# Optimization experiments

Hardware: AMD Instinct MI355X
Metric: run time of the kernel (lower is better)

Reference implementation:

```python
import jax, jax.numpy as jnp
import numpy as np
from jax import lax

PC_RANGE = (-54.0, -54.0, -5.0, 54.0, 54.0, 3.0)
HEIGHTS = (-1.0, 0.0, 1.0)  # all within [z_min, z_max]
IMG_H, IMG_W = 256.0, 704.0  # batch_input_shape of the camera image
BN_EPS = 1e-5


def setup_inputs() -> dict:
    key = jax.random.key(0)
    ks = jax.random.split(key, 11)
    d = {}
    d['radar_bev'] = jax.random.normal(ks[0], (2, 384, 180, 180), jnp.float32)
    d['img_feat'] = jax.random.normal(ks[1], (2, 256, 64, 176), jnp.float32)
    d['lidar2img'] = jax.random.normal(ks[2], (2, 3, 4), jnp.float32)
    d['w1'] = jax.random.normal(ks[3], (384, 256, 1, 1), jnp.float32) * 0.05
    d['bn1'] = jax.random.uniform(ks[4], (4, 384), jnp.float32, 0.1, 1.0)
    d['w2'] = jax.random.normal(ks[5], (384, 384, 3, 3), jnp.float32) * 0.02
    d['bn2'] = jax.random.uniform(ks[6], (4, 384), jnp.float32, 0.1, 1.0)
    d['wf1'] = jax.random.normal(ks[7], (384, 768, 3, 3), jnp.float32) * 0.02
    d['bnf1'] = jax.random.uniform(ks[8], (4, 384), jnp.float32, 0.1, 1.0)
    d['wf2'] = jax.random.normal(ks[9], (384, 384, 3, 3), jnp.float32) * 0.02
    d['bnf2'] = jax.random.uniform(ks[10], (4, 384), jnp.float32, 0.1, 1.0)
    return d


def _conv(x, w, pad):
    return lax.conv_general_dilated(x, w, (1, 1), [(pad, pad), (pad, pad)],
                                    dimension_numbers=('NCHW', 'OIHW', 'NCHW'))


def _bn_relu(x, p):
    g, b, m, v = p[0], p[1], p[2], p[3]
    y = (x - m[:, None, None]) * (g[:, None, None] / jnp.sqrt(v[:, None, None] + BN_EPS)) + b[:, None, None]
    return jax.nn.relu(y)


def _bilinear_sample(img, gx, gy):
    # img: [C,H,W]; gx,gy: [N] normalized coords in grid_sample convention
    # (align_corners=False, padding_mode='zeros')
    C, H, W = img.shape
    ix = ((gx + 1.0) * W - 1.0) * 0.5
    iy = ((gy + 1.0) * H - 1.0) * 0.5
    x0 = jnp.floor(ix); y0 = jnp.floor(iy)
    wx1 = ix - x0; wx0 = 1.0 - wx1
    wy1 = iy - y0; wy0 = 1.0 - wy1

    def corner(xc, yc, w):
        inb = (xc >= 0) & (xc < W) & (yc >= 0) & (yc < H)
        xi = jnp.clip(xc, 0, W - 1).astype(jnp.int32)
        yi = jnp.clip(yc, 0, H - 1).astype(jnp.int32)
        return img[:, yi, xi] * (w * inb)[None, :]

    return (corner(x0, y0, wx0 * wy0) + corner(x0 + 1, y0, wx1 * wy0)
            + corner(x0, y0 + 1, wx0 * wy1) + corner(x0 + 1, y0 + 1, wx1 * wy1))


def reference(radar_bev, img_feat, lidar2img, w1, bn1, w2, bn2, wf1, bnf1, wf2, bnf2):
    B, _, bev_h, bev_w = radar_bev.shape
    x_min, y_min, z_min, x_max, y_max, z_max = PC_RANGE
    xs = jnp.linspace(x_min, x_max, bev_w + 1, dtype=jnp.float32)[:-1] + (x_max - x_min) / bev_w * 0.5
    ys = jnp.linspace(y_min, y_max, bev_h + 1, dtype=jnp.float32)[:-1] + (y_max - y_min) / bev_h * 0.5
    gy, gx = jnp.meshgrid(ys, xs, indexing='ij')  # [bev_h, bev_w]
    zs = jnp.asarray(HEIGHTS, jnp.float32)
    Z = zs.shape[0]
    # points: [Z, bev_h, bev_w, 4] -> [N, 4]
    pts = jnp.stack([jnp.broadcast_to(gx, (Z, bev_h, bev_w)),
                     jnp.broadcast_to(gy, (Z, bev_h, bev_w)),
                     jnp.broadcast_to(zs[:, None, None], (Z, bev_h, bev_w)),
                     jnp.ones((Z, bev_h, bev_w), jnp.float32)], axis=-1).reshape(-1, 4)
    # project: [B, N, 3]
    proj = jnp.einsum('nk,bjk->bnj', pts, lidar2img)
    depth = jnp.maximum(proj[:, :, 2], 1e-5)
    px = proj[:, :, 0] / depth
    py = proj[:, :, 1] / depth
    norm_x = px / IMG_W * 2.0 - 1.0
    norm_y = py / IMG_H * 2.0 - 1.0
    sampled = jax.vmap(_bilinear_sample)(img_feat, norm_x, norm_y)  # [B, C, N]
    valid = ((px >= 0) & (px < IMG_W) & (py >= 0) & (py < IMG_H)
             & (proj[:, :, 2] > 1e-5)).astype(jnp.float32)  # [B, N]
    C = img_feat.shape[1]
    sampled = sampled.reshape(B, C, Z, bev_h, bev_w)
    valid = valid.reshape(B, 1, Z, bev_h, bev_w)
    image_bev = (sampled * valid).sum(axis=2) / jnp.maximum(valid.sum(axis=2), 1.0)
    # image_bev_encoder: 1x1 conv -> BN -> ReLU -> 3x3 conv -> BN -> ReLU
    h = _bn_relu(_conv(image_bev, w1, 0), bn1)
    h = _bn_relu(_conv(h, w2, 1), bn2)
    # bev_fusion on concat(radar, image_bev)
    f = jnp.concatenate([radar_bev, h], axis=1)
    f = _bn_relu(_conv(f, wf1, 1), bnf1)
    f = _bn_relu(_conv(f, wf2, 1), bnf2)
    return f
```

## Files before the change

kernel.cpp:

```cpp
#include <hip/hip_runtime.h>
#include <hip/hip_bf16.h>

#define BEV 180
#define NPOS (BEV * BEV)
#define MTOT (2 * NPOS)
#define IH 64
#define IW 176
#define CIMG 256

typedef __attribute__((ext_vector_type(8))) short bf16x8;
typedef __attribute__((ext_vector_type(4))) float f32x4;

__device__ __forceinline__ void gload_lds16(const void* g, void* l) {
  __builtin_amdgcn_global_load_lds(
      (const __attribute__((address_space(1))) void*)g,
      (__attribute__((address_space(3))) void*)l, 16, 0, 0);
}

__global__ void k_zero(unsigned long long* p) { p[threadIdx.x] = 0ULL; }

template <typename OT>
__device__ __forceinline__ OT conv_out(float v);
template <>
__device__ __forceinline__ float conv_out<float>(float v) { return v; }
template <>
__device__ __forceinline__ __hip_bfloat16 conv_out<__hip_bfloat16>(float v) { return __float2bfloat16(v); }

template <typename OT>
__global__ void k_transpose(const float* __restrict__ in, OT* __restrict__ out, int R, int CL) {
  __shared__ float tile[32][33];
  const float* inb = in + (size_t)blockIdx.z * R * CL;
  OT* outb = out + (size_t)blockIdx.z * R * CL;
  int c0 = blockIdx.x * 32, r0 = blockIdx.y * 32;
  int tx = threadIdx.x, ty = threadIdx.y;
#pragma unroll
  for (int i = 0; i < 32; i += 8) {
    int r = r0 + ty + i, c = c0 + tx;
    tile[ty + i][tx] = (r < R && c < CL) ? inb[(size_t)r * CL + c] : 0.f;
  }
  __syncthreads();
#pragma unroll
  for (int i = 0; i < 32; i += 8) {
    int c = c0 + ty + i, r = r0 + tx;
    if (c < CL && r < R) outb[(size_t)c * R + r] = conv_out<OT>(tile[tx][ty + i]);
  }
}

__global__ void k_sample(const float* __restrict__ imgT, const float* __restrict__ l2i,
                         __hip_bfloat16* __restrict__ out) {
  int blk = blockIdx.x;
  int b = blk / NPOS, rem = blk - b * NPOS;
  int hy = rem / BEV, wx = rem - hy * BEV;
  int c = threadIdx.x;
  float gx = -54.f + 0.3f + 0.6f * (float)wx;
  float gy = -54.f + 0.3f + 0.6f * (float)hy;
  const float* L = l2i + b * 12;
  const float* img = imgT + (size_t)b * (IH * IW * CIMG);
  float acc = 0.f, vcnt = 0.f;
#pragma unroll
  for (int zi = 0; zi < 3; ++zi) {
    float z = (float)(zi - 1);
    float p0 = L[0] * gx + L[1] * gy + L[2] * z + L[3];
    float p1 = L[4] * gx + L[5] * gy + L[6] * z + L[7];
    float p2 = L[8] * gx + L[9] * gy + L[10] * z + L[11];
    float d = fmaxf(p2, 1e-5f);
    float px = p0 / d, py = p1 / d;
    if (px >= 0.f && px < 704.f && py >= 0.f && py < 256.f && p2 > 1e-5f) {
      vcnt += 1.f;
      float ix = px * 0.25f - 0.5f, iy = py * 0.25f - 0.5f;
      float xf = floorf(ix), yf = floorf(iy);
      float wx1 = ix - xf, wy1 = iy - yf;
      float wx0 = 1.f - wx1, wy0 = 1.f - wy1;
      int x0 = (int)xf, y0 = (int)yf;
      int x1 = x0 + 1, y1 = y0 + 1;
      bool bx0 = (unsigned)x0 < IW, bx1 = (unsigned)x1 < IW;
      bool by0 = (unsigned)y0 < IH, by1 = (unsigned)y1 < IH;
      float s = 0.f;
      if (bx0 && by0) s += wx0 * wy0 * img[((size_t)y0 * IW + x0) * CIMG + c];
      if (bx1 && by0) s += wx1 * wy0 * img[((size_t)y0 * IW + x1) * CIMG + c];
      if (bx0 && by1) s += wx0 * wy1 * img[((size_t)y1 * IW + x0) * CIMG + c];
      if (bx1 && by1) s += wx1 * wy1 * img[((size_t)y1 * IW + x1) * CIMG + c];
      acc += s;
    }
  }
  out[(size_t)blk * CIMG + c] = __float2bfloat16(acc / fmaxf(vcnt, 1.f));
}

__global__ void k_packw(const float* __restrict__ w, __hip_bfloat16* __restrict__ wp,
                        int Co, int Ci, int T) {
  size_t idx = (size_t)blockIdx.x * 256 + threadIdx.x;
  size_t tot = (size_t)Co * Ci * T;
  if (idx >= tot) return;
  int ci = (int)(idx % Ci);
  size_t r = idx / Ci;
  int co = (int)(r % Co);
  int tap = (int)(r / Co);
  wp[idx] = __float2bfloat16(w[((size_t)co * Ci + ci) * T + tap]);
}

__global__ void k_packbn(const float* __restrict__ bn, float* __restrict__ sb, int C) {
  int i = blockIdx.x * blockDim.x + threadIdx.x;
  if (i >= C) return;
  float g = bn[i], b = bn[C + i], m = bn[2 * C + i], v = bn[3 * C + i];
  float s = g / sqrtf(v + 1e-5f);
  sb[i] = s;
  sb[C + i] = b - m * s;
}

__global__ __launch_bounds__(256, 2) void k_conv(
    const __hip_bfloat16* __restrict__ x0, const __hip_bfloat16* __restrict__ x1,
    int cin0, int cin1,
    const __hip_bfloat16* __restrict__ wp, const float* __restrict__ sb,
    int taps, int isFinal,
    __hip_bfloat16* __restrict__ obf, float* __restrict__ of32,
    const __hip_bfloat16* __restrict__ zp) {
  const int Cout = 384;
  __shared__ __hip_bfloat16 As[352 * 64];
  __shared__ __hip_bfloat16 Bs[2][128 * 64];
  const int t = threadIdx.x;
  const int w = t >> 6, l = t & 63;
  const int bid = blockIdx.x;
  const int b = bid / 144;
  const int rr = bid - b * 144;
  const int y0 = (rr / 12) * 16;
  const int x0c = (rr - (rr / 12) * 12) * 16;
  const int n0 = blockIdx.y * 128;
  const int cinTot = cin0 + cin1;
  const size_t tapStride = (size_t)Cout * cinTot * 2;
  const int nA0 = cin0 >> 6, nA1 = cin1 >> 6, nA = nA0 + nA1;
  const int P = nA * taps;

  const int baseRow = t >> 3;
  const int cb = ((t & 7) ^ (baseRow & 7)) * 16;
  int posIdx[11];
  unsigned okMask = 0;
#pragma unroll
  for (int j = 0; j < 11; ++j) {
    int row = j * 32 + baseRow;
    int yy = row / 18, xx = row - yy * 18;
    int ys = y0 - 1 + yy, xg = x0c - 1 + xx;
    if (row < 324 && (unsigned)ys < 180u && (unsigned)xg < 180u) okMask |= (1u << j);
    posIdx[j] = b * NPOS + ys * BEV + xg;
  }
  size_t bOff[4];
#pragma unroll
  for (int j = 0; j < 4; ++j)
    bOff[j] = (size_t)(n0 + j * 32 + baseRow) * (size_t)(cinTot * 2) + (size_t)cb;

  auto issueA = [&](int kc) {
    int s1 = (kc >= nA0);
    int kcw = kc - (s1 ? nA0 : 0);
    const char* xb = s1 ? (const char*)x1 : (const char*)x0;
    size_t cinB = (size_t)(s1 ? cin1 : cin0) * 2;
    size_t ko = (size_t)kcw * 128 + (size_t)cb;
    char* dst = (char*)As + w * 1024;
#pragma unroll
    for (int j = 0; j < 11; ++j) {
      const char* src = ((okMask >> j) & 1) ? (xb + (size_t)posIdx[j] * cinB + ko)
                                            : (const char*)zp;
      gload_lds16(src, dst + j * 4096);
    }
  };
  auto issueB = [&](int q, int kc, int tq) {
    int s1 = (kc >= nA0);
    int kcw = kc - (s1 ? nA0 : 0);
    int segoff = s1 ? cin0 : 0;
    const char* wt = (const char*)wp + (size_t)tq * tapStride + (size_t)(segoff + kcw * 64) * 2;
    char* dst = (char*)Bs[q & 1] + w * 1024;
#pragma unroll
    for (int j = 0; j < 4; ++j) gload_lds16(wt + bOff[j], dst + j * 4096);
  };

  f32x4 acc[8][4];
#pragma unroll
  for (int mi = 0; mi < 8; ++mi)
#pragma unroll
    for (int ni = 0; ni < 4; ++ni) acc[mi][ni] = f32x4{0.f, 0.f, 0.f, 0.f};

  const int wq = w >> 1;
  const int wn = (w & 1) * 64;
  const int xl = l & 15, kq = l >> 4;

  issueA(0);
  issueB(0, 0, 0);

  int kc = 0, tap = 0;
  for (int p = 0; p < P; ++p) {
    if (p + 1 < P) {
      int tq = tap + 1, kn = kc;
      if (tq == taps) { tq = 0; ++kn; }
      issueB(p + 1, kn, tq);
      asm volatile("s_waitcnt vmcnt(4)" ::: "memory");
    } else {
      asm volatile("s_waitcnt vmcnt(0)" ::: "memory");
    }
    __builtin_amdgcn_s_barrier();
    asm volatile("" ::: "memory");

    const int dy = (taps == 9) ? (tap / 3 - 1) : 0;
    const int dx = (taps == 9) ? (tap - (tap / 3) * 3 - 1) : 0;
    const int sRow0 = (wq * 8 + dy + 1) * 18 + xl + dx + 1;
    const char* bLds = (const char*)Bs[p & 1];
    __builtin_amdgcn_s_setprio(1);
#pragma unroll
    for (int ks = 0; ks < 2; ++ks) {
      const int g = ks * 4 + kq;
      bf16x8 af[8], bfr[4];
#pragma unroll
      for (int mi = 0; mi < 8; ++mi) {
        int s = sRow0 + mi * 18;
        af[mi] = *(const bf16x8*)((const char*)As + s * 128 + ((g ^ (s & 7)) * 16));
      }
#pragma unroll
      for (int ni = 0; ni < 4; ++ni) {
        int rB = wn + ni * 16 + xl;
        bfr[ni] = *(const bf16x8*)(bLds + rB * 128 + ((g ^ (rB & 7)) * 16));
      }
#pragma unroll
      for (int mi = 0; mi < 8; ++mi)
#pragma unroll
        for (int ni = 0; ni < 4; ++ni)
          acc[mi][ni] = __builtin_amdgcn_mfma_f32_16x16x32_bf16(af[mi], bfr[ni], acc[mi][ni], 0, 0, 0);
    }
    __builtin_amdgcn_s_setprio(0);
    asm volatile("" ::: "memory");
    __builtin_amdgcn_s_barrier();

    if (tap == taps - 1 && kc + 1 < nA) issueA(kc + 1);
    if (++tap == taps) { tap = 0; ++kc; }
  }

  float sc[4], bi[4];
#pragma unroll
  for (int ni = 0; ni < 4; ++ni) {
    int cc = n0 + wn + ni * 16 + xl;
    sc[ni] = sb[cc];
    bi[ni] = sb[Cout + cc];
  }
#pragma unroll
  for (int mi = 0; mi < 8; ++mi) {
    int y = y0 + wq * 8 + mi;
    if (y >= BEV) continue;
#pragma unroll
    for (int j = 0; j < 4; ++j) {
      int x = x0c + kq * 4 + j;
      if (x >= BEV) continue;
      int pp = b * NPOS + y * BEV + x;
#pragma unroll
      for (int ni = 0; ni < 4; ++ni) {
        int cc = n0 + wn + ni * 16 + xl;
        float v = fmaxf(acc[mi][ni][j] * sc[ni] + bi[ni], 0.f);
        if (isFinal) {
          of32[((size_t)(b * Cout + cc)) * NPOS + (size_t)y * BEV + x] = v;
        } else {
          obf[(size_t)pp * Cout + cc] = __float2bfloat16(v);
        }
      }
    }
  }
}

extern "C" void kernel_launch(void* const* d_in, const int* in_sizes, int n_in,
                              void* d_out, int out_size, void* d_ws, size_t ws_size,
                              hipStream_t stream) {
  const float* radar = (const float*)d_in[0];
  const float* imgf = (const float*)d_in[1];
  const float* l2i = (const float*)d_in[2];
  const float* w1 = (const float*)d_in[3];
  const float* bn1 = (const float*)d_in[4];
  const float* w2 = (const float*)d_in[5];
  const float* bn2 = (const float*)d_in[6];
  const float* wf1 = (const float*)d_in[7];
  const float* bnf1 = (const float*)d_in[8];
  const float* wf2 = (const float*)d_in[9];
  const float* bnf2 = (const float*)d_in[10];

  char* ws = (char*)d_ws;
  size_t off = 0;
  auto alloc = [&](size_t bytes) {
    char* p = ws + off;
    off += (bytes + 255) & ~(size_t)255;
    return p;
  };
  char* zp = alloc(4096);
  char* imgT = alloc((size_t)2 * IH * IW * CIMG * 4);
  char* ibev = alloc((size_t)MTOT * CIMG * 2);
  char* radarT = imgT;
  char* h1 = alloc((size_t)MTOT * 384 * 2);
  char* h2 = alloc((size_t)MTOT * 384 * 2);
  char* f1 = h1;
  char* wp1 = alloc((size_t)1 * 384 * 256 * 2);
  char* wp2 = alloc((size_t)9 * 384 * 384 * 2);
  char* wpf1 = alloc((size_t)9 * 384 * 768 * 2);
  char* wpf2 = alloc((size_t)9 * 384 * 384 * 2);
  char* sb1 = alloc(2 * 384 * 4);
  char* sb2 = alloc(2 * 384 * 4);
  char* sbf1 = alloc(2 * 384 * 4);
  char* sbf2 = alloc(2 * 384 * 4);

  k_zero<<<1, 512, 0, stream>>>((unsigned long long*)zp);

  dim3 tb(32, 8);
  k_transpose<float><<<dim3((IH * IW + 31) / 32, (CIMG + 31) / 32, 2), tb, 0, stream>>>(
      imgf, (float*)imgT, CIMG, IH * IW);

  auto packw = [&](const float* src, char* dst, int Co, int Ci, int T) {
    size_t tot = (size_t)Co * Ci * T;
    k_packw<<<(unsigned)((tot + 255) / 256), 256, 0, stream>>>(src, (__hip_bfloat16*)dst, Co, Ci, T);
  };
  packw(w1, wp1, 384, 256, 1);
  packw(w2, wp2, 384, 384, 9);
  packw(wf1, wpf1, 384, 768, 9);
  packw(wf2, wpf2, 384, 384, 9);
  k_packbn<<<2, 256, 0, stream>>>(bn1, (float*)sb1, 384);
  k_packbn<<<2, 256, 0, stream>>>(bn2, (float*)sb2, 384);
  k_packbn<<<2, 256, 0, stream>>>(bnf1, (float*)sbf1, 384);
  k_packbn<<<2, 256, 0, stream>>>(bnf2, (float*)sbf2, 384);

  k_sample<<<MTOT, 256, 0, stream>>>((const float*)imgT, l2i, (__hip_bfloat16*)ibev);

  dim3 cg(288, 3);
  k_conv<<<cg, 256, 0, stream>>>((const __hip_bfloat16*)ibev, nullptr, 256, 0,
                                 (const __hip_bfloat16*)wp1, (const float*)sb1, 1, 0,
                                 (__hip_bfloat16*)h1, nullptr, (const __hip_bfloat16*)zp);
  k_transpose<__hip_bfloat16><<<dim3((NPOS + 31) / 32, (384 + 31) / 32, 2), tb, 0, stream>>>(
      radar, (__hip_bfloat16*)radarT, 384, NPOS);
  k_conv<<<cg, 256, 0, stream>>>((const __hip_bfloat16*)h1, nullptr, 384, 0,
                                 (const __hip_bfloat16*)wp2, (const float*)sb2, 9, 0,
                                 (__hip_bfloat16*)h2, nullptr, (const __hip_bfloat16*)zp);
  k_conv<<<cg, 256, 0, stream>>>((const __hip_bfloat16*)radarT, (const __hip_bfloat16*)h2, 384, 384,
                                 (const __hip_bfloat16*)wpf1, (const float*)sbf1, 9, 0,
                                 (__hip_bfloat16*)f1, nullptr, (const __hip_bfloat16*)zp);
  k_conv<<<cg, 256, 0, stream>>>((const __hip_bfloat16*)f1, nullptr, 384, 0,
                                 (const __hip_bfloat16*)wpf2, (const float*)sbf2, 9, 1,
                                 nullptr, (float*)d_out, (const __hip_bfloat16*)zp);
}
```

Baseline: 940.0 us.

## Use bf16 image features and cut per-iteration barriers in conv pipeline

```diff
diff --git a/kernel.cpp b/kernel.cpp
--- a/kernel.cpp
+++ b/kernel.cpp
@@ -46,7 +46,7 @@
   }
 }
 
-__global__ void k_sample(const float* __restrict__ imgT, const float* __restrict__ l2i,
+__global__ void k_sample(const __hip_bfloat16* __restrict__ imgT, const float* __restrict__ l2i,
                          __hip_bfloat16* __restrict__ out) {
   int blk = blockIdx.x;
   int b = blk / NPOS, rem = blk - b * NPOS;
@@ -55,7 +55,7 @@
   float gx = -54.f + 0.3f + 0.6f * (float)wx;
   float gy = -54.f + 0.3f + 0.6f * (float)hy;
   const float* L = l2i + b * 12;
-  const float* img = imgT + (size_t)b * (IH * IW * CIMG);
+  const __hip_bfloat16* img = imgT + (size_t)b * (IH * IW * CIMG);
   float acc = 0.f, vcnt = 0.f;
 #pragma unroll
   for (int zi = 0; zi < 3; ++zi) {
@@ -76,10 +76,10 @@
       bool bx0 = (unsigned)x0 < IW, bx1 = (unsigned)x1 < IW;
       bool by0 = (unsigned)y0 < IH, by1 = (unsigned)y1 < IH;
       float s = 0.f;
-      if (bx0 && by0) s += wx0 * wy0 * img[((size_t)y0 * IW + x0) * CIMG + c];
-      if (bx1 && by0) s += wx1 * wy0 * img[((size_t)y0 * IW + x1) * CIMG + c];
-      if (bx0 && by1) s += wx0 * wy1 * img[((size_t)y1 * IW + x0) * CIMG + c];
-      if (bx1 && by1) s += wx1 * wy1 * img[((size_t)y1 * IW + x1) * CIMG + c];
+      if (bx0 && by0) s += wx0 * wy0 * __bfloat162float(img[((size_t)y0 * IW + x0) * CIMG + c]);
+      if (bx1 && by0) s += wx1 * wy0 * __bfloat162float(img[((size_t)y0 * IW + x1) * CIMG + c]);
+      if (bx0 && by1) s += wx0 * wy1 * __bfloat162float(img[((size_t)y1 * IW + x0) * CIMG + c]);
+      if (bx1 && by1) s += wx1 * wy1 * __bfloat162float(img[((size_t)y1 * IW + x1) * CIMG + c]);
       acc += s;
     }
   }
@@ -107,11 +107,12 @@
   sb[C + i] = b - m * s;
 }
 
+template <int TAPS>
 __global__ __launch_bounds__(256, 2) void k_conv(
     const __hip_bfloat16* __restrict__ x0, const __hip_bfloat16* __restrict__ x1,
     int cin0, int cin1,
     const __hip_bfloat16* __restrict__ wp, const float* __restrict__ sb,
-    int taps, int isFinal,
+    int isFinal,
     __hip_bfloat16* __restrict__ obf, float* __restrict__ of32,
     const __hip_bfloat16* __restrict__ zp) {
   const int Cout = 384;
@@ -128,7 +129,7 @@
   const int cinTot = cin0 + cin1;
   const size_t tapStride = (size_t)Cout * cinTot * 2;
   const int nA0 = cin0 >> 6, nA1 = cin1 >> 6, nA = nA0 + nA1;
-  const int P = nA * taps;
+  const int P = nA * TAPS;
 
   const int baseRow = t >> 3;
   const int cb = ((t & 7) ^ (baseRow & 7)) * 16;
@@ -186,19 +187,17 @@
 
   int kc = 0, tap = 0;
   for (int p = 0; p < P; ++p) {
+    asm volatile("s_waitcnt vmcnt(0)" ::: "memory");
+    __builtin_amdgcn_s_barrier();
+    asm volatile("" ::: "memory");
     if (p + 1 < P) {
       int tq = tap + 1, kn = kc;
-      if (tq == taps) { tq = 0; ++kn; }
+      if (tq == TAPS) { tq = 0; ++kn; }
       issueB(p + 1, kn, tq);
-      asm volatile("s_waitcnt vmcnt(4)" ::: "memory");
-    } else {
-      asm volatile("s_waitcnt vmcnt(0)" ::: "memory");
-    }
-    __builtin_amdgcn_s_barrier();
-    asm volatile("" ::: "memory");
-
-    const int dy = (taps == 9) ? (tap / 3 - 1) : 0;
-    const int dx = (taps == 9) ? (tap - (tap / 3) * 3 - 1) : 0;
+    }
+
+    const int dy = (TAPS == 9) ? (tap / 3 - 1) : 0;
+    const int dx = (TAPS == 9) ? (tap - (tap / 3) * 3 - 1) : 0;
     const int sRow0 = (wq * 8 + dy + 1) * 18 + xl + dx + 1;
     const char* bLds = (const char*)Bs[p & 1];
     __builtin_amdgcn_s_setprio(1);
@@ -224,10 +223,12 @@
     }
     __builtin_amdgcn_s_setprio(0);
     asm volatile("" ::: "memory");
-    __builtin_amdgcn_s_barrier();
-
-    if (tap == taps - 1 && kc + 1 < nA) issueA(kc + 1);
-    if (++tap == taps) { tap = 0; ++kc; }
+
+    if (tap == TAPS - 1 && kc + 1 < nA) {
+      __builtin_amdgcn_s_barrier();
+      issueA(kc + 1);
+    }
+    if (++tap == TAPS) { tap = 0; ++kc; }
   }
 
   float sc[4], bi[4];
@@ -301,8 +302,8 @@
   k_zero<<<1, 512, 0, stream>>>((unsigned long long*)zp);
 
   dim3 tb(32, 8);
-  k_transpose<float><<<dim3((IH * IW + 31) / 32, (CIMG + 31) / 32, 2), tb, 0, stream>>>(
-      imgf, (float*)imgT, CIMG, IH * IW);
+  k_transpose<__hip_bfloat16><<<dim3((IH * IW + 31) / 32, (CIMG + 31) / 32, 2), tb, 0, stream>>>(
+      imgf, (__hip_bfloat16*)imgT, CIMG, IH * IW);
 
   auto packw = [&](const float* src, char* dst, int Co, int Ci, int T) {
     size_t tot = (size_t)Co * Ci * T;
@@ -317,21 +318,21 @@
   k_packbn<<<2, 256, 0, stream>>>(bnf1, (float*)sbf1, 384);
   k_packbn<<<2, 256, 0, stream>>>(bnf2, (float*)sbf2, 384);
 
-  k_sample<<<MTOT, 256, 0, stream>>>((const float*)imgT, l2i, (__hip_bfloat16*)ibev);
+  k_sample<<<MTOT, 256, 0, stream>>>((const __hip_bfloat16*)imgT, l2i, (__hip_bfloat16*)ibev);
 
   dim3 cg(288, 3);
-  k_conv<<<cg, 256, 0, stream>>>((const __hip_bfloat16*)ibev, nullptr, 256, 0,
-                                 (const __hip_bfloat16*)wp1, (const float*)sb1, 1, 0,
-                                 (__hip_bfloat16*)h1, nullptr, (const __hip_bfloat16*)zp);
+  k_conv<1><<<cg, 256, 0, stream>>>((const __hip_bfloat16*)ibev, nullptr, 256, 0,
+                                    (const __hip_bfloat16*)wp1, (const float*)sb1, 0,
+                                    (__hip_bfloat16*)h1, nullptr, (const __hip_bfloat16*)zp);
   k_transpose<__hip_bfloat16><<<dim3((NPOS + 31) / 32, (384 + 31) / 32, 2), tb, 0, stream>>>(
       radar, (__hip_bfloat16*)radarT, 384, NPOS);
-  k_conv<<<cg, 256, 0, stream>>>((const __hip_bfloat16*)h1, nullptr, 384, 0,
-                                 (const __hip_bfloat16*)wp2, (const float*)sb2, 9, 0,
-                                 (__hip_bfloat16*)h2, nullptr, (const __hip_bfloat16*)zp);
-  k_conv<<<cg, 256, 0, stream>>>((const __hip_bfloat16*)radarT, (const __hip_bfloat16*)h2, 384, 384,
-                                 (const __hip_bfloat16*)wpf1, (const float*)sbf1, 9, 0,
-                                 (__hip_bfloat16*)f1, nullptr, (const __hip_bfloat16*)zp);
-  k_conv<<<cg, 256, 0, stream>>>((const __hip_bfloat16*)f1, nullptr, 384, 0,
-                                 (const __hip_bfloat16*)wpf2, (const float*)sbf2, 9, 1,
-                                 nullptr, (float*)d_out, (const __hip_bfloat16*)zp);
-}
+  k_conv<9><<<cg, 256, 0, stream>>>((const __hip_bfloat16*)h1, nullptr, 384, 0,
+                                    (const __hip_bfloat16*)wp2, (const float*)sb2, 0,
+                                    (__hip_bfloat16*)h2, nullptr, (const __hip_bfloat16*)zp);
+  k_conv<9><<<cg, 256, 0, stream>>>((const __hip_bfloat16*)radarT, (const __hip_bfloat16*)h2, 384, 384,
+                                    (const __hip_bfloat16*)wpf1, (const float*)sbf1, 0,
+                                    (__hip_bfloat16*)f1, nullptr, (const __hip_bfloat16*)zp);
+  k_conv<9><<<cg, 256, 0, stream>>>((const __hip_bfloat16*)f1, nullptr, 384, 0,
+                                    (const __hip_bfloat16*)wpf2, (const float*)sbf2, 1,
+                                    nullptr, (float*)d_out, (const __hip_bfloat16*)zp);
+}
```

After: 934.0 us. No clear change (-0.6%).
